# Kernel tuning notes

Measured on AMD Instinct MI355X. Metric: run time of the kernel, lower is better.

Reference implementation:

```python
import jax, jax.numpy as jnp
import numpy as np

TEMP = 13.544
EPS = 1e-5  # BatchNorm2d default eps


def setup_inputs() -> dict:
    key = jax.random.key(0)
    k1, = jax.random.split(key, 1)
    N, S, E = 16, 1024, 512
    x = jax.random.normal(k1, (N, S, E), dtype=jnp.float32)
    gamma = jnp.ones((1,), dtype=jnp.float32)   # BatchNorm2d(1).weight
    beta = jnp.zeros((1,), dtype=jnp.float32)   # BatchNorm2d(1).bias
    return {"x": x, "gamma": gamma, "beta": beta}


def reference(x, gamma, beta):
    # Pairwise squared L2 distances via GEMM identity:
    # ||a-b||^2 = ||a||^2 + ||b||^2 - 2 a.b   (symmetric, matches the
    # original broadcast diff+square+sum without the O(S^2 E) intermediate)
    sq = jnp.sum(x * x, axis=-1)                    # (N, S)
    gram = jnp.einsum('bse,bte->bst', x, x)         # (N, S, S)
    d = sq[:, :, None] + sq[:, None, :] - 2.0 * gram  # (N, S, S)
    d = jnp.maximum(d, 0.0)                          # numerical floor (exact math is >= 0)

    # BatchNorm2d(1) in training mode: stats over all elements of the single channel
    d = d[:, None, :, :]                             # (N, 1, S, S)
    mean = jnp.mean(d)
    var = jnp.mean((d - mean) ** 2)                  # biased variance, as torch uses for normalization
    d_hat = (d - mean) * jax.lax.rsqrt(var + EPS)
    out = d_hat * gamma.reshape(1, 1, 1, 1) + beta.reshape(1, 1, 1, 1)

    # softmax(-out / 13.544) over last dim
    return jax.nn.softmax(-out / TEMP, axis=-1)      # (N, 1, S, S)
```

## Files before the change

### kernel.cpp

```cpp
#include <hip/hip_runtime.h>
#include <hip/hip_bf16.h>


#define S_DIM 1024
#define E_DIM 512
#define NBATCH 16
#define TEMP_C 13.544

typedef __attribute__((ext_vector_type(4))) float f32x4;
typedef __attribute__((ext_vector_type(8))) short bf16x8;
typedef __attribute__((ext_vector_type(8))) _Float16 f16x8;

__device__ inline unsigned pkbf(float lo, float hi) {
  unsigned a = __float_as_uint(lo), b = __float_as_uint(hi);
  a = (a + 0x7FFFu + ((a >> 16) & 1u)) >> 16;
  b = (b + 0x7FFFu + ((b >> 16) & 1u)) & 0xFFFF0000u;
  return b | a;
}

__global__ __launch_bounds__(256) void sqcvt(const float* __restrict__ x,
                                             ushort* __restrict__ xb16,
                                             float* __restrict__ sq,
                                             double* __restrict__ sums) {
  const int wave = threadIdx.x >> 6, lane = threadIdx.x & 63;
  const int xcd = blockIdx.x & 7, li = blockIdx.x >> 3;
  const size_t row = (size_t)xcd * 2048 + (size_t)li * 4 + wave;
  const float4* xr = reinterpret_cast<const float4*>(x + row * E_DIM);
  float4 a = xr[lane * 2], b = xr[lane * 2 + 1];
  uint4 p;
  p.x = pkbf(a.x, a.y); p.y = pkbf(a.z, a.w);
  p.z = pkbf(b.x, b.y); p.w = pkbf(b.z, b.w);
  *reinterpret_cast<uint4*>(xb16 + row * E_DIM + lane * 8) = p;
  float s = a.x*a.x + a.y*a.y + a.z*a.z + a.w*a.w +
            b.x*b.x + b.y*b.y + b.z*b.z + b.w*b.w;
#pragma unroll
  for (int o = 32; o > 0; o >>= 1) s += __shfl_xor(s, o);
  if (lane == 0) sq[row] = s;
  if (blockIdx.x == 0 && threadIdx.x == 0) { sums[0] = 0.0; sums[1] = 0.0; }
}

template <int MODE>
__global__ __launch_bounds__(512) void gram8(const ushort* __restrict__ xb16,
                                             const float* __restrict__ sq,
                                             float* __restrict__ dout,
                                             _Float16* __restrict__ dp,
                                             double* __restrict__ sums) {
  __shared__ double red[16];

  const int tid = threadIdx.x, wave = tid >> 6, lane = tid & 63;
  const int wr = wave >> 2, wc = wave & 3;

  const int bid = blockIdx.x;
  const int xcd = bid & 7, j = bid >> 3;
  const int b = xcd * 2 + (j >> 4);
  const int tile = j & 15;
  const int tr = tile >> 2, tc = tile & 3;

  const ushort* xb = xb16 + (size_t)b * (S_DIM * E_DIM);
  const int rowA0 = tr * 256, rowB0 = tc * 256;

  const char* Abase = (const char*)(xb + (size_t)(rowA0 + wr * 128 + (lane & 15)) * E_DIM)
                      + (lane >> 4) * 16;
  const char* Bbase = (const char*)(xb + (size_t)(rowB0 + wc * 64 + (lane & 15)) * E_DIM)
                      + (lane >> 4) * 16;

  f32x4 acc[8][4] = {};

#pragma unroll 2
  for (int ks = 0; ks < E_DIM / 32; ++ks) {
    const int ko = ks * 64;
    bf16x8 af[8], bfr[4];
#pragma unroll
    for (int m = 0; m < 8; ++m)
      af[m] = *reinterpret_cast<const bf16x8*>(Abase + (size_t)m * 16 * 1024 + ko);
#pragma unroll
    for (int n = 0; n < 4; ++n)
      bfr[n] = *reinterpret_cast<const bf16x8*>(Bbase + (size_t)n * 16 * 1024 + ko);
#pragma unroll
    for (int m = 0; m < 8; ++m)
#pragma unroll
      for (int n = 0; n < 4; ++n)
        acc[m][n] = __builtin_amdgcn_mfma_f32_16x16x32_bf16(af[m], bfr[n], acc[m][n], 0, 0, 0);
  }

  const float* sqb = sq + b * S_DIM;
  double sd = 0.0, sd2 = 0.0;
#pragma unroll
  for (int m = 0; m < 8; ++m) {
    int gr0 = tr * 256 + wr * 128 + m * 16 + ((lane >> 4) << 2);
    float sqr0 = sqb[gr0], sqr1 = sqb[gr0 + 1], sqr2 = sqb[gr0 + 2], sqr3 = sqb[gr0 + 3];
#pragma unroll
    for (int n = 0; n < 4; ++n) {
      int gc = tc * 256 + wc * 64 + n * 16 + (lane & 15);
      float sqc = sqb[gc];
      float d0 = fmaxf(sqr0 + sqc - 2.0f * acc[m][n][0], 0.0f);
      float d1 = fmaxf(sqr1 + sqc - 2.0f * acc[m][n][1], 0.0f);
      float d2 = fmaxf(sqr2 + sqc - 2.0f * acc[m][n][2], 0.0f);
      float d3 = fmaxf(sqr3 + sqc - 2.0f * acc[m][n][3], 0.0f);
      if (MODE == 0) {
        float* dbase = dout + (size_t)b * S_DIM * S_DIM;
        dbase[(size_t)(gr0 + 0) * S_DIM + gc] = d0;
        dbase[(size_t)(gr0 + 1) * S_DIM + gc] = d1;
        dbase[(size_t)(gr0 + 2) * S_DIM + gc] = d2;
        dbase[(size_t)(gr0 + 3) * S_DIM + gc] = d3;
      } else {
        _Float16* dbase = dp + (size_t)b * S_DIM * S_DIM;
        dbase[(size_t)(gr0 + 0) * S_DIM + gc] = (_Float16)(d0 - sqr0);
        dbase[(size_t)(gr0 + 1) * S_DIM + gc] = (_Float16)(d1 - sqr1);
        dbase[(size_t)(gr0 + 2) * S_DIM + gc] = (_Float16)(d2 - sqr2);
        dbase[(size_t)(gr0 + 3) * S_DIM + gc] = (_Float16)(d3 - sqr3);
      }
      sd += (double)d0 + (double)d1 + (double)d2 + (double)d3;
      sd2 += (double)d0 * d0 + (double)d1 * d1 + (double)d2 * d2 + (double)d3 * d3;
    }
  }
#pragma unroll
  for (int o = 32; o > 0; o >>= 1) {
    sd += __shfl_xor(sd, o);
    sd2 += __shfl_xor(sd2, o);
  }
  if (lane == 0) { red[wave] = sd; red[8 + wave] = sd2; }
  __syncthreads();
  if (tid == 0) {
    double t1 = 0.0, t2 = 0.0;
#pragma unroll
    for (int w = 0; w < 8; ++w) { t1 += red[w]; t2 += red[8 + w]; }
    atomicAdd(&sums[0], t1);
    atomicAdd(&sums[1], t2);
  }
}

__device__ inline float ln_scale(const double* sums, const float* gamma) {
  constexpr double invN = 1.0 / (16.0 * 1024.0 * 1024.0);
  double mean = sums[0] * invN;
  double var = sums[1] * invN - mean * mean;
  return (float)(-((double)gamma[0]) / (sqrt(var + 1e-5) * TEMP_C));
}

__global__ __launch_bounds__(256) void softmax_f32(float* __restrict__ d,
                                                   const double* __restrict__ sums,
                                                   const float* __restrict__ gamma) {
  const int wave = threadIdx.x >> 6, lane = threadIdx.x & 63;
  const int xcd = blockIdx.x & 7, li = blockIdx.x >> 3;
  const size_t row = (size_t)xcd * 2048 + (size_t)li * 4 + wave;
  const float scale = ln_scale(sums, gamma);
  float4* r4 = reinterpret_cast<float4*>(d + row * S_DIM);
  float4 v[4];
#pragma unroll
  for (int i = 0; i < 4; ++i) v[i] = r4[lane + 64 * i];
  float l[16];
#pragma unroll
  for (int i = 0; i < 4; ++i) {
    l[4*i+0] = scale * v[i].x; l[4*i+1] = scale * v[i].y;
    l[4*i+2] = scale * v[i].z; l[4*i+3] = scale * v[i].w;
  }
  float mx = l[0];
#pragma unroll
  for (int i = 1; i < 16; ++i) mx = fmaxf(mx, l[i]);
#pragma unroll
  for (int o = 32; o > 0; o >>= 1) mx = fmaxf(mx, __shfl_xor(mx, o));
  const float L2E = 1.4426950408889634f;
  float e[16], s = 0.f;
#pragma unroll
  for (int i = 0; i < 16; ++i) { e[i] = exp2f((l[i] - mx) * L2E); s += e[i]; }
#pragma unroll
  for (int o = 32; o > 0; o >>= 1) s += __shfl_xor(s, o);
  float inv = 1.0f / s;
#pragma unroll
  for (int i = 0; i < 4; ++i)
    r4[lane + 64 * i] = make_float4(e[4*i]*inv, e[4*i+1]*inv, e[4*i+2]*inv, e[4*i+3]*inv);
}

__global__ __launch_bounds__(256) void softmax_f16(const _Float16* __restrict__ dp,
                                                   float* __restrict__ out,
                                                   const double* __restrict__ sums,
                                                   const float* __restrict__ gamma) {
  const int wave = threadIdx.x >> 6, lane = threadIdx.x & 63;
  const int xcd = blockIdx.x & 7, li = blockIdx.x >> 3;
  const size_t row = (size_t)xcd * 2048 + (size_t)li * 4 + wave;
  const float scale = ln_scale(sums, gamma);
  const f16x8* r8 = reinterpret_cast<const f16x8*>(dp + row * S_DIM);
  f16x8 h0 = r8[lane * 2], h1 = r8[lane * 2 + 1];
  float l[16];
#pragma unroll
  for (int i = 0; i < 8; ++i) { l[i] = scale * (float)h0[i]; l[8 + i] = scale * (float)h1[i]; }
  float mx = l[0];
#pragma unroll
  for (int i = 1; i < 16; ++i) mx = fmaxf(mx, l[i]);
#pragma unroll
  for (int o = 32; o > 0; o >>= 1) mx = fmaxf(mx, __shfl_xor(mx, o));
  const float L2E = 1.4426950408889634f;
  float e[16], s = 0.f;
#pragma unroll
  for (int i = 0; i < 16; ++i) { e[i] = exp2f((l[i] - mx) * L2E); s += e[i]; }
#pragma unroll
  for (int o = 32; o > 0; o >>= 1) s += __shfl_xor(s, o);
  float inv = 1.0f / s;
  float4* o4 = reinterpret_cast<float4*>(out + row * S_DIM);
#pragma unroll
  for (int i = 0; i < 4; ++i)
    o4[lane * 4 + i] = make_float4(e[4*i]*inv, e[4*i+1]*inv, e[4*i+2]*inv, e[4*i+3]*inv);
}

extern "C" void kernel_launch(void* const* d_in, const int* in_sizes, int n_in,
                              void* d_out, int out_size, void* d_ws, size_t ws_size,
                              hipStream_t stream) {
  const float* x = (const float*)d_in[0];
  const float* gamma = (const float*)d_in[1];
  float* out = (float*)d_out;
  double* sums = (double*)d_ws;
  float* sq = (float*)((char*)d_ws + 256);
  ushort* xb16 = (ushort*)((char*)d_ws + 256 + 65536);
  _Float16* dp = (_Float16*)((char*)d_ws + 256 + 65536 +
                             (size_t)NBATCH * S_DIM * E_DIM * 2);
  const size_t need_b = 256 + 65536 + (size_t)NBATCH * S_DIM * E_DIM * 2;
  const size_t need_a = need_b + (size_t)NBATCH * S_DIM * S_DIM * 2;

  sqcvt<<<dim3(NBATCH * S_DIM / 4), dim3(256), 0, stream>>>(x, xb16, sq, sums);
  if (ws_size >= need_a) {
    gram8<1><<<dim3(256), dim3(512), 0, stream>>>(xb16, sq, out, dp, sums);
    softmax_f16<<<dim3(NBATCH * S_DIM / 4), dim3(256), 0, stream>>>(dp, out, sums, gamma);
  } else {
    gram8<0><<<dim3(256), dim3(512), 0, stream>>>(xb16, sq, out, dp, sums);
    softmax_f32<<<dim3(NBATCH * S_DIM / 4), dim3(256), 0, stream>>>(out, sums, gamma);
  }
}
```

Measured before the change: 175.0 us.

## Stage Gram GEMM operands through double-buffered swizzled LDS with async global loads

The Gram kernel used to read bf16 operand fragments straight from global memory into registers. It now copies 256x64 A and B k-slices into XOR-swizzled, double-buffered LDS using global_load_lds. The next slice is prefetched while MFMAs run on the current one, with barriers and raised wave priority around the MFMA phases. The aim is to hide global load latency and make operand reuse explicit across waves, at the cost of 128KB of LDS and extra barrier synchronisation.

```diff
diff --git a/kernel.cpp b/kernel.cpp
--- a/kernel.cpp
+++ b/kernel.cpp
@@ -16,6 +16,12 @@
   a = (a + 0x7FFFu + ((a >> 16) & 1u)) >> 16;
   b = (b + 0x7FFFu + ((b >> 16) & 1u)) & 0xFFFF0000u;
   return b | a;
+}
+
+__device__ inline void gload16(const void* g, void* l) {
+  __builtin_amdgcn_global_load_lds(
+      (const __attribute__((address_space(1))) unsigned*)g,
+      (__attribute__((address_space(3))) unsigned*)l, 16, 0, 0);
 }
 
 __global__ __launch_bounds__(256) void sqcvt(const float* __restrict__ x,
@@ -40,11 +46,13 @@
 }
 
 template <int MODE>
-__global__ __launch_bounds__(512) void gram8(const ushort* __restrict__ xb16,
+__global__ __launch_bounds__(512) void gram9(const ushort* __restrict__ xb16,
                                              const float* __restrict__ sq,
                                              float* __restrict__ dout,
                                              _Float16* __restrict__ dp,
                                              double* __restrict__ sums) {
+  __shared__ ushort lA[2][2][128][64];
+  __shared__ ushort lB[2][2][128][64];
   __shared__ double red[16];
 
   const int tid = threadIdx.x, wave = tid >> 6, lane = tid & 63;
@@ -59,28 +67,83 @@
   const ushort* xb = xb16 + (size_t)b * (S_DIM * E_DIM);
   const int rowA0 = tr * 256, rowB0 = tc * 256;
 
-  const char* Abase = (const char*)(xb + (size_t)(rowA0 + wr * 128 + (lane & 15)) * E_DIM)
-                      + (lane >> 4) * 16;
-  const char* Bbase = (const char*)(xb + (size_t)(rowB0 + wc * 64 + (lane & 15)) * E_DIM)
-                      + (lane >> 4) * 16;
+  int eA[2], eB[2];
+#pragma unroll
+  for (int i = 0; i < 2; ++i) {
+    int p = i * 512 + tid;
+    int r = p >> 3;
+    int sl = (p & 7) ^ (r & 7);
+    eA[i] = (rowA0 + r) * E_DIM + sl * 8;
+    eB[i] = (rowB0 + r) * E_DIM + sl * 8;
+  }
+
+  auto stage = [&](int kt, int idx) {
+    const int buf = kt & 1, h = idx & 1;
+    const int off = h * 128 * E_DIM + kt * 64;
+    if (idx < 2) {
+      char* dst = (char*)&lA[buf][h][0][0];
+      gload16(xb + eA[0] + off, dst + tid * 16);
+      gload16(xb + eA[1] + off, dst + 8192 + tid * 16);
+    } else {
+      char* dst = (char*)&lB[buf][h][0][0];
+      gload16(xb + eB[0] + off, dst + tid * 16);
+      gload16(xb + eB[1] + off, dst + 8192 + tid * 16);
+    }
+  };
 
   f32x4 acc[8][4] = {};
-
-#pragma unroll 2
-  for (int ks = 0; ks < E_DIM / 32; ++ks) {
-    const int ko = ks * 64;
-    bf16x8 af[8], bfr[4];
-#pragma unroll
-    for (int m = 0; m < 8; ++m)
-      af[m] = *reinterpret_cast<const bf16x8*>(Abase + (size_t)m * 16 * 1024 + ko);
-#pragma unroll
-    for (int n = 0; n < 4; ++n)
-      bfr[n] = *reinterpret_cast<const bf16x8*>(Bbase + (size_t)n * 16 * 1024 + ko);
-#pragma unroll
-    for (int m = 0; m < 8; ++m)
-#pragma unroll
-      for (int n = 0; n < 4; ++n)
-        acc[m][n] = __builtin_amdgcn_mfma_f32_16x16x32_bf16(af[m], bfr[n], acc[m][n], 0, 0, 0);
+  bf16x8 af[4][2], bfr[2][2];
+
+  stage(0, 0); stage(0, 1); stage(0, 2); stage(0, 3);
+
+#pragma unroll 1
+  for (int kt = 0; kt < 8; ++kt) {
+    const char* la = (const char*)&lA[kt & 1][0][0][0];
+    const char* lb = (const char*)&lB[kt & 1][0][0][0];
+#pragma unroll
+    for (int ph = 0; ph < 4; ++ph) {
+      const int mq = ph >> 1, nq = ph & 1;
+      if (kt < 7) stage(kt + 1, ph);
+      if (ph == 0) {
+        if (kt < 7) asm volatile("s_waitcnt vmcnt(2)" ::: "memory");
+        else        asm volatile("s_waitcnt vmcnt(0)" ::: "memory");
+      }
+      __builtin_amdgcn_s_barrier();
+      __builtin_amdgcn_sched_barrier(0);
+
+      if (nq == 0) {
+#pragma unroll
+        for (int mf = 0; mf < 4; ++mf)
+#pragma unroll
+          for (int ks = 0; ks < 2; ++ks) {
+            int row = wr * 128 + mq * 64 + mf * 16 + (lane & 15);
+            int half = row >> 7, r = row & 127;
+            int sl = (ks * 4 + (lane >> 4)) ^ (r & 7);
+            af[mf][ks] = *reinterpret_cast<const bf16x8*>(la + half * 16384 + r * 128 + sl * 16);
+          }
+      }
+#pragma unroll
+      for (int nf = 0; nf < 2; ++nf)
+#pragma unroll
+        for (int ks = 0; ks < 2; ++ks) {
+          int row = wc * 64 + nq * 32 + nf * 16 + (lane & 15);
+          int half = row >> 7, r = row & 127;
+          int sl = (ks * 4 + (lane >> 4)) ^ (r & 7);
+          bfr[nf][ks] = *reinterpret_cast<const bf16x8*>(lb + half * 16384 + r * 128 + sl * 16);
+        }
+
+      __builtin_amdgcn_s_setprio(1);
+#pragma unroll
+      for (int ks = 0; ks < 2; ++ks)
+#pragma unroll
+        for (int mf = 0; mf < 4; ++mf)
+#pragma unroll
+          for (int nf = 0; nf < 2; ++nf)
+            acc[mq * 4 + mf][nq * 2 + nf] = __builtin_amdgcn_mfma_f32_16x16x32_bf16(
+                af[mf][ks], bfr[nf][ks], acc[mq * 4 + mf][nq * 2 + nf], 0, 0, 0);
+      __builtin_amdgcn_s_setprio(0);
+      __builtin_amdgcn_s_barrier();
+    }
   }
 
   const float* sqb = sq + b * S_DIM;
@@ -218,10 +281,10 @@
 
   sqcvt<<<dim3(NBATCH * S_DIM / 4), dim3(256), 0, stream>>>(x, xb16, sq, sums);
   if (ws_size >= need_a) {
-    gram8<1><<<dim3(256), dim3(512), 0, stream>>>(xb16, sq, out, dp, sums);
+    gram9<1><<<dim3(256), dim3(512), 0, stream>>>(xb16, sq, out, dp, sums);
     softmax_f16<<<dim3(NBATCH * S_DIM / 4), dim3(256), 0, stream>>>(dp, out, sums, gamma);
   } else {
-    gram8<0><<<dim3(256), dim3(512), 0, stream>>>(xb16, sq, out, dp, sums);
+    gram9<0><<<dim3(256), dim3(512), 0, stream>>>(xb16, sq, out, dp, sums);
     softmax_f32<<<dim3(NBATCH * S_DIM / 4), dim3(256), 0, stream>>>(out, sums, gamma);
   }
 }
```

Result: faster. 148.5 us (-15.1%).
